# Performance work log

Hardware: AMD Instinct MI355X
Metric: run time of the kernel (lower is better)

## Reference

```python
import jax, jax.numpy as jnp
import numpy as np

# ---- constants (match init_kwargs) ----
H = 16            # bit depth of location codes
TP = 8            # number of parallel location dims
N = 1 << H        # location magnitude bound
N_K = 2
N_C = 2 * H * N_K + 1   # 65 candidate locations per token
T = 512           # T_train
N_TTNBR = 64
K_VOCAB = 128
S = N_TTNBR + K_VOCAB   # 192
D = 256           # dim_eu
TEMP = 0.05


def cos_similarity(c1, c2):
    """CritiGraph frexp-based cosine: sign product * (1 - bitlength(|a|^|b| + 1)/h)."""
    sg = (2 * (c1 >= 0).astype(jnp.int32) - 1) * (2 * (c2 >= 0).astype(jnp.int32) - 1)
    x = jnp.abs(c1) ^ jnp.abs(c2)
    _, e = jnp.frexp((x + 1).astype(jnp.float32))  # exponent == bit_length(x+1)
    return sg.astype(jnp.float32) * (1.0 - e.astype(jnp.float32) / H)


def setup_inputs() -> dict:
    key = jax.random.key(0)
    ks = jax.random.split(key, 8)
    loc = lambda k, shape: jax.random.randint(k, shape, 1 - N, N, dtype=jnp.int32)
    return {
        "cur_tar": jax.random.randint(ks[0], (T,), 0, K_VOCAB, dtype=jnp.int32),
        "cnc_loc": loc(ks[1], (T, N_C, TP)),
        "sta_loc": loc(ks[2], (T, TP)),
        "ttn_loc": loc(ks[3], (T, N_TTNBR, TP)),
        "voc_loc": loc(ks[4], (T, K_VOCAB, TP)),
        "sta_emb": 0.1 * jax.random.normal(ks[5], (T, D), dtype=jnp.float32),
        "ttn_emb": 0.1 * jax.random.normal(ks[6], (T, N_TTNBR, D), dtype=jnp.float32),
        "voc_emb": 0.1 * jax.random.normal(ks[7], (T, K_VOCAB, D), dtype=jnp.float32),
    }


def reference(cur_tar, cnc_loc, sta_loc, ttn_loc, voc_loc, sta_emb, ttn_emb, voc_emb):
    # positives = dynamic neighbors ++ sampled vocab
    pos_loc = jnp.concatenate([ttn_loc, voc_loc], axis=1)      # (T, S, TP) int32
    pos_emb = jnp.concatenate([ttn_emb, voc_emb], axis=1)      # (T, S, D)

    # Euclidean-space logits
    eu_val = 20.0 * TEMP * jnp.einsum('td,tsd->ts', sta_emb, pos_emb)  # (T, S)

    # CT-space similarities
    cos_sp = cos_similarity(sta_loc[:, None, :], pos_loc)      # (T, S, TP)
    cos_sum = cos_sp.sum(axis=-1)                              # (T, S)
    # candidate location swapped into each track d (ct_val_triton math)
    cos_cp = cos_similarity(cnc_loc[:, None, :, :], pos_loc[:, :, None, :])  # (T, S, N_C, TP)
    ct_val = (cos_sum[:, :, None, None] - cos_sp[:, :, None, :] + cos_cp) / TP \
             * (20.0 * TEMP)                                   # (T, S, N_C, TP)

    # KL(eu || ct) over the dynamic neighbors
    logits_ct_dyn = ct_val[:, :N_TTNBR]                        # (T, Nn, N_C, TP)
    logits_eu_dyn = eu_val[:, :N_TTNBR]                        # (T, Nn)
    p_eu = jax.nn.softmax(logits_eu_dyn, axis=1)
    lp_eu = jax.nn.log_softmax(logits_eu_dyn, axis=1)
    lp_ct = jax.nn.log_softmax(logits_ct_dyn, axis=1)
    loss_dyn_dyn = (p_eu[:, :, None, None] * (lp_eu[:, :, None, None] - lp_ct)).sum(axis=1)  # (T, N_C, TP)

    # cross-entropy over the sampled vocab
    logits_ct_sta = ct_val[:, N_TTNBR:] / TEMP                 # (T, K, N_C, TP)
    logits_flat = logits_ct_sta.reshape(T, K_VOCAB, N_C * TP)
    log_probs = jax.nn.log_softmax(logits_flat, axis=1)        # (T, K, N_C*TP)
    idx = jnp.broadcast_to(cur_tar[:, None, None].astype(jnp.int32), (T, 1, N_C * TP))
    target_lp = jnp.take_along_axis(log_probs, idx, axis=1)[:, 0, :]  # (T, N_C*TP)
    loss_dyn_sta = -target_lp.reshape(T, N_C, TP)              # (T, N_C, TP)

    return loss_dyn_dyn, loss_dyn_sta
```

## Files before the change

### kernel.cpp

```cpp
#include <hip/hip_runtime.h>


#define Tn   512
#define NC   65
#define TPd  8
#define NTn  64
#define KV   128
#define Sn   192
#define Dn   256
#define OUT1 (Tn * NC * TPd)

#define LOG2E 1.44269504088896340736f
#define LN2   0.69314718055994530942f
#define K1D (0.0625f * 0.125f * LOG2E)
#define K0D (-0.125f * LOG2E)
#define K1S (0.0625f * 2.5f * LOG2E)
#define K0S (-2.5f * LOG2E)

__device__ __forceinline__ float exp2_fast(float x) {
#if __has_builtin(__builtin_amdgcn_exp2f)
    return __builtin_amdgcn_exp2f(x);
#else
    return exp2f(x);
#endif
}
__device__ __forceinline__ int pack_loc(int v) {
    return (v < 0) ? (int)(0x80000000u | (unsigned)(-v)) : v;
}
__device__ __forceinline__ float asf(int v) { return __int_as_float(v); }

__device__ __forceinline__ float cos_cc(int y, float k1, float k0) {
    int   x  = (y & 0x7fffffff) + 1;
    float cc = fmaf((float)__clz(x), k1, k0);
    return __int_as_float(__float_as_int(cc) ^ (y & 0x80000000));
}

__global__ __launch_bounds__(256, 2) void critigraph_kernel(
    const int*   __restrict__ cur_tar,
    const int*   __restrict__ cnc_loc,
    const int*   __restrict__ sta_loc,
    const int*   __restrict__ ttn_loc,
    const int*   __restrict__ voc_loc,
    const float* __restrict__ sta_emb,
    const float* __restrict__ ttn_emb,
    float*       __restrict__ out)
{
    __shared__ int4  s_dyn4[NTn * TPd];
    __shared__ int2  s_sta2[KV * TPd];
    __shared__ int   s_cnc[NC * TPd];
    __shared__ int   s_staloc[TPd];
    __shared__ float s_csum[Sn];
    __shared__ float s_eu[NTn];
    __shared__ float s_peu[NTn];
    __shared__ float s_dotbase[TPd];
    __shared__ float s_kl;

    const int t   = blockIdx.x;
    const int tid = threadIdx.x;

    if (tid < TPd) s_staloc[tid] = pack_loc(sta_loc[t * TPd + tid]);
    for (int i = tid; i < NC * TPd; i += 256)
        s_cnc[i] = pack_loc(cnc_loc[t * NC * TPd + i]);
    __syncthreads();

    const int mysta = s_staloc[tid & 7];
    float mysp[6];
    #pragma unroll
    for (int k = 0; k < 6; ++k) {
        int i = tid + 256 * k;
        int s = i >> 3;
        int v = (s < NTn) ? ttn_loc[t * NTn * TPd + i]
                          : voc_loc[t * KV * TPd + (i - NTn * TPd)];
        int packed = pack_loc(v);
        int y = packed ^ mysta;
        int x = (y & 0x7fffffff) + 1;
        float c = fmaf((float)__clz(x), 0.0625f, -1.0f);
        c = __int_as_float(__float_as_int(c) ^ (y & 0x80000000));
        mysp[k] = c;
        if (s < NTn) s_dyn4[i].x = packed;
        else         s_sta2[i - NTn * TPd].x = packed;
        float v8 = c;
        v8 += __shfl_xor(v8, 1);
        v8 += __shfl_xor(v8, 2);
        v8 += __shfl_xor(v8, 4);
        if ((tid & 7) == 0) s_csum[s] = v8;
    }
    {
        const int r = tid >> 2, q = tid & 3;
        const float4* A = (const float4*)(sta_emb + (size_t)t * Dn);
        const float4* B = (const float4*)(ttn_emb + ((size_t)t * NTn + r) * Dn);
        float acc = 0.f;
        #pragma unroll
        for (int k = 0; k < 16; ++k) {
            float4 a = A[k * 4 + q];
            float4 b = B[k * 4 + q];
            acc += a.x * b.x + a.y * b.y + a.z * b.z + a.w * b.w;
        }
        acc += __shfl_xor(acc, 1);
        acc += __shfl_xor(acc, 2);
        if (q == 0) s_eu[r] = acc;
    }
    __syncthreads();

    #pragma unroll
    for (int k = 0; k < 6; ++k) {
        int i = tid + 256 * k;
        int s = i >> 3;
        float sc = (s < NTn) ? (0.125f * LOG2E) : (2.5f * LOG2E);
        float b2 = (s_csum[s] - mysp[k]) * sc;
        if (s < NTn) s_dyn4[i].y = __float_as_int(b2);
        else         s_sta2[i - NTn * TPd].y = __float_as_int(b2);
    }
    if (tid < 64) {
        float e  = s_eu[tid];
        float mx = e;
        #pragma unroll
        for (int m = 1; m < 64; m <<= 1) mx = fmaxf(mx, __shfl_xor(mx, m));
        float ex = __expf(e - mx);
        float z  = ex;
        #pragma unroll
        for (int m = 1; m < 64; m <<= 1) z += __shfl_xor(z, m);
        float pe = ex / z;
        s_peu[tid] = pe;
        float kls = pe * ((e - mx) - __logf(z));
        #pragma unroll
        for (int m = 1; m < 64; m <<= 1) kls += __shfl_xor(kls, m);
        if (tid == 0) s_kl = kls;
    }
    __syncthreads();

    #pragma unroll
    for (int k = 0; k < 2; ++k) {
        int i = tid + 256 * k;
        s_dyn4[i].z = __float_as_int(s_peu[i >> 3]);
    }
    if (tid < 64) {
        int g = tid & 7, j = tid >> 3;
        float a = 0.f;
        #pragma unroll
        for (int k = 0; k < 8; ++k) {
            int s = 8 * j + k;
            a = fmaf(s_peu[s], asf(s_dyn4[s * TPd + g].y), a);
        }
        #pragma unroll
        for (int m = 8; m < 64; m <<= 1) a += __shfl_xor(a, m);
        if (tid < TPd) s_dotbase[g] = a;
    }
    __syncthreads();

    const int p     = tid & 7;
    const int acnc1 = s_cnc[tid];
    const int acnc2 = s_cnc[tid + 256];
    const int tar   = cur_tar[t];
    const float kl  = s_kl;
    const float dtb = s_dotbase[p];

    float sumA = 0.f, dotA = 0.f, sumB = 0.f, dotB = 0.f;
    #pragma unroll 16
    for (int s = 0; s < NTn; ++s) {
        int4  ab = s_dyn4[s * TPd + p];
        float bb = asf(ab.y);
        float pe = asf(ab.z);
        float ccA = cos_cc(ab.x ^ acnc1, K1D, K0D);
        sumA += exp2_fast(bb + ccA);
        dotA  = fmaf(pe, ccA, dotA);
        float ccB = cos_cc(ab.x ^ acnc2, K1D, K0D);
        sumB += exp2_fast(bb + ccB);
        dotB  = fmaf(pe, ccB, dotB);
    }
    float s2A = 0.f, s2B = 0.f;
    #pragma unroll 16
    for (int v = 0; v < KV; ++v) {
        int2  ab = s_sta2[v * TPd + p];
        float bb = asf(ab.y);
        s2A += exp2_fast(bb + cos_cc(ab.x ^ acnc1, K1S, K0S));
        s2B += exp2_fast(bb + cos_cc(ab.x ^ acnc2, K1S, K0S));
    }
    {
        int2  tt = s_sta2[tar * TPd + p];
        float bt = asf(tt.y);
        float tA = bt + cos_cc(tt.x ^ acnc1, K1S, K0S);
        float tB = bt + cos_cc(tt.x ^ acnc2, K1S, K0S);
        float* od = out + (size_t)t * NC * TPd;
        float* os = out + OUT1 + (size_t)t * NC * TPd;
        od[tid]       = kl + LN2 * (__log2f(sumA) - (dtb + dotA));
        od[tid + 256] = kl + LN2 * (__log2f(sumB) - (dtb + dotB));
        os[tid]       = LN2 * (__log2f(s2A) - tA);
        os[tid + 256] = LN2 * (__log2f(s2B) - tB);
    }

    {
        const int w    = tid >> 6;
        const int lane = tid & 63;
        const int half = lane >> 5;
        const int sub  = lane & 31;
        const int pt   = 2 * w + half;
        const int acnct = s_cnc[512 + pt];
        float sumd = 0.f, dotd = 0.f, sums = 0.f;
        #pragma unroll
        for (int k = 0; k < 2; ++k) {
            int4 ab = s_dyn4[(sub + 32 * k) * TPd + pt];
            float cc = cos_cc(ab.x ^ acnct, K1D, K0D);
            sumd += exp2_fast(asf(ab.y) + cc);
            dotd  = fmaf(asf(ab.z), cc, dotd);
        }
        #pragma unroll
        for (int k = 0; k < 4; ++k) {
            int2 ab = s_sta2[(sub + 32 * k) * TPd + pt];
            sums += exp2_fast(asf(ab.y) + cos_cc(ab.x ^ acnct, K1S, K0S));
        }
        #pragma unroll
        for (int m = 1; m < 32; m <<= 1) {
            sumd += __shfl_xor(sumd, m);
            dotd += __shfl_xor(dotd, m);
            sums += __shfl_xor(sums, m);
        }
        if (sub == 0) {
            int2  tt = s_sta2[tar * TPd + pt];
            float tT = asf(tt.y) + cos_cc(tt.x ^ acnct, K1S, K0S);
            out[(size_t)t * NC * TPd + 512 + pt] =
                kl + LN2 * (__log2f(sumd) - (s_dotbase[pt] + dotd));
            out[OUT1 + (size_t)t * NC * TPd + 512 + pt] =
                LN2 * (__log2f(sums) - tT);
        }
    }
}

extern "C" void kernel_launch(void* const* d_in, const int* in_sizes, int n_in,
                              void* d_out, int out_size, void* d_ws, size_t ws_size,
                              hipStream_t stream) {
    (void)in_sizes; (void)n_in; (void)d_ws; (void)ws_size; (void)out_size;
    const int*   cur_tar = (const int*)  d_in[0];
    const int*   cnc_loc = (const int*)  d_in[1];
    const int*   sta_loc = (const int*)  d_in[2];
    const int*   ttn_loc = (const int*)  d_in[3];
    const int*   voc_loc = (const int*)  d_in[4];
    const float* sta_emb = (const float*)d_in[5];
    const float* ttn_emb = (const float*)d_in[6];
    critigraph_kernel<<<Tn, 256, 0, stream>>>(cur_tar, cnc_loc, sta_loc, ttn_loc,
                                              voc_loc, sta_emb, ttn_emb, (float*)d_out);
}
```

Before: 142.8 us.

## Replace per-element exp2 with shared lookup table and double block size

Factors exp2(b + cc) into exp2(b)*exp2(cc). The base exp2 is precomputed once per position, and exp2(cc) comes from a small shared-memory table indexed by clz and sign. The table is replicated 32 ways to avoid bank conflicts. Blocks grow to 512 threads so each thread handles one candidate column instead of two. This removes transcendental ops from the inner loops, at the cost of extra shared memory, table-fill work and table lookups, and it changes occupancy. The target log-prob term is recomputed from the cosine terms because stored values are now exponentiated.

```diff
diff --git a/kernel.cpp b/kernel.cpp
--- a/kernel.cpp
+++ b/kernel.cpp
@@ -9,11 +9,11 @@
 #define Sn   192
 #define Dn   256
 #define OUT1 (Tn * NC * TPd)
+#define TABN 34
+#define TABR (TABN * 32)
 
 #define LOG2E 1.44269504088896340736f
 #define LN2   0.69314718055994530942f
-#define K1D (0.0625f * 0.125f * LOG2E)
-#define K0D (-0.125f * LOG2E)
 #define K1S (0.0625f * 2.5f * LOG2E)
 #define K0S (-2.5f * LOG2E)
 
@@ -29,13 +29,18 @@
 }
 __device__ __forceinline__ float asf(int v) { return __int_as_float(v); }
 
-__device__ __forceinline__ float cos_cc(int y, float k1, float k0) {
-    int   x  = (y & 0x7fffffff) + 1;
-    float cc = fmaf((float)__clz(x), k1, k0);
-    return __int_as_float(__float_as_int(cc) ^ (y & 0x80000000));
-}
-
-__global__ __launch_bounds__(256, 2) void critigraph_kernel(
+__device__ __forceinline__ float cos_raw(int y) {
+    int   x = (y & 0x7fffffff) + 1;
+    float c = fmaf((float)__clz(x), 0.0625f, -1.0f);
+    return __int_as_float(__float_as_int(c) ^ (y & 0x80000000));
+}
+__device__ __forceinline__ int tab_idx(int y) {
+    int x = (y & 0x7fffffff) + 1;
+    int u = __clz(x) - 15;
+    return u * 2 + (int)(((unsigned)y) >> 31);
+}
+
+__global__ __launch_bounds__(512, 4) void critigraph_kernel(
     const int*   __restrict__ cur_tar,
     const int*   __restrict__ cnc_loc,
     const int*   __restrict__ sta_loc,
@@ -47,6 +52,7 @@
 {
     __shared__ int4  s_dyn4[NTn * TPd];
     __shared__ int2  s_sta2[KV * TPd];
+    __shared__ float s_tab[3 * TABR];
     __shared__ int   s_cnc[NC * TPd];
     __shared__ int   s_staloc[TPd];
     __shared__ float s_csum[Sn];
@@ -59,23 +65,31 @@
     const int tid = threadIdx.x;
 
     if (tid < TPd) s_staloc[tid] = pack_loc(sta_loc[t * TPd + tid]);
-    for (int i = tid; i < NC * TPd; i += 256)
+    for (int i = tid; i < NC * TPd; i += 512)
         s_cnc[i] = pack_loc(cnc_loc[t * NC * TPd + i]);
+    for (int i = tid; i < TABR; i += 512) {
+        int   idx = i >> 5;
+        int   clz = 15 + (idx >> 1);
+        float mag = (float)clz * 0.0625f - 1.0f;
+        float sgn = (idx & 1) ? -1.f : 1.f;
+        float ccd = sgn * mag * (0.125f * LOG2E);
+        float ccs = sgn * mag * (2.5f * LOG2E);
+        s_tab[i]            = exp2_fast(ccd);
+        s_tab[i + TABR]     = ccd;
+        s_tab[i + 2 * TABR] = exp2_fast(ccs);
+    }
     __syncthreads();
 
     const int mysta = s_staloc[tid & 7];
-    float mysp[6];
+    float mysp[3];
     #pragma unroll
-    for (int k = 0; k < 6; ++k) {
-        int i = tid + 256 * k;
+    for (int k = 0; k < 3; ++k) {
+        int i = tid + 512 * k;
         int s = i >> 3;
         int v = (s < NTn) ? ttn_loc[t * NTn * TPd + i]
                           : voc_loc[t * KV * TPd + (i - NTn * TPd)];
         int packed = pack_loc(v);
-        int y = packed ^ mysta;
-        int x = (y & 0x7fffffff) + 1;
-        float c = fmaf((float)__clz(x), 0.0625f, -1.0f);
-        c = __int_as_float(__float_as_int(c) ^ (y & 0x80000000));
+        float c = cos_raw(packed ^ mysta);
         mysp[k] = c;
         if (s < NTn) s_dyn4[i].x = packed;
         else         s_sta2[i - NTn * TPd].x = packed;
@@ -86,30 +100,35 @@
         if ((tid & 7) == 0) s_csum[s] = v8;
     }
     {
-        const int r = tid >> 2, q = tid & 3;
+        const int r = tid >> 3, q = tid & 7;
         const float4* A = (const float4*)(sta_emb + (size_t)t * Dn);
         const float4* B = (const float4*)(ttn_emb + ((size_t)t * NTn + r) * Dn);
         float acc = 0.f;
         #pragma unroll
-        for (int k = 0; k < 16; ++k) {
-            float4 a = A[k * 4 + q];
-            float4 b = B[k * 4 + q];
+        for (int k = 0; k < 8; ++k) {
+            float4 a = A[k * 8 + q];
+            float4 b = B[k * 8 + q];
             acc += a.x * b.x + a.y * b.y + a.z * b.z + a.w * b.w;
         }
         acc += __shfl_xor(acc, 1);
         acc += __shfl_xor(acc, 2);
+        acc += __shfl_xor(acc, 4);
         if (q == 0) s_eu[r] = acc;
     }
     __syncthreads();
 
     #pragma unroll
-    for (int k = 0; k < 6; ++k) {
-        int i = tid + 256 * k;
+    for (int k = 0; k < 3; ++k) {
+        int i = tid + 512 * k;
         int s = i >> 3;
-        float sc = (s < NTn) ? (0.125f * LOG2E) : (2.5f * LOG2E);
-        float b2 = (s_csum[s] - mysp[k]) * sc;
-        if (s < NTn) s_dyn4[i].y = __float_as_int(b2);
-        else         s_sta2[i - NTn * TPd].y = __float_as_int(b2);
+        if (s < NTn) {
+            float b2 = (s_csum[s] - mysp[k]) * (0.125f * LOG2E);
+            s_dyn4[i].y = __float_as_int(exp2_fast(b2));
+            s_dyn4[i].w = __float_as_int(b2);
+        } else {
+            float b2 = (s_csum[s] - mysp[k]) * (2.5f * LOG2E);
+            s_sta2[i - NTn * TPd].y = __float_as_int(exp2_fast(b2));
+        }
     }
     if (tid < 64) {
         float e  = s_eu[tid];
@@ -129,18 +148,14 @@
     }
     __syncthreads();
 
-    #pragma unroll
-    for (int k = 0; k < 2; ++k) {
-        int i = tid + 256 * k;
-        s_dyn4[i].z = __float_as_int(s_peu[i >> 3]);
-    }
+    s_dyn4[tid].z = __float_as_int(s_peu[tid >> 3]);
     if (tid < 64) {
         int g = tid & 7, j = tid >> 3;
         float a = 0.f;
         #pragma unroll
         for (int k = 0; k < 8; ++k) {
             int s = 8 * j + k;
-            a = fmaf(s_peu[s], asf(s_dyn4[s * TPd + g].y), a);
+            a = fmaf(s_peu[s], asf(s_dyn4[s * TPd + g].w), a);
         }
         #pragma unroll
         for (int m = 8; m < 64; m <<= 1) a += __shfl_xor(a, m);
@@ -148,80 +163,80 @@
     }
     __syncthreads();
 
-    const int p     = tid & 7;
-    const int acnc1 = s_cnc[tid];
-    const int acnc2 = s_cnc[tid + 256];
-    const int tar   = cur_tar[t];
-    const float kl  = s_kl;
-    const float dtb = s_dotbase[p];
-
-    float sumA = 0.f, dotA = 0.f, sumB = 0.f, dotB = 0.f;
+    const int   p    = tid & 7;
+    const int   acnc = s_cnc[tid];
+    const int   tar  = cur_tar[t];
+    const float kl   = s_kl;
+    const float dtb  = s_dotbase[p];
+    const float* tb  = s_tab + (tid & 31);
+
+    float sum = 0.f, dot = 0.f;
     #pragma unroll 16
     for (int s = 0; s < NTn; ++s) {
-        int4  ab = s_dyn4[s * TPd + p];
-        float bb = asf(ab.y);
-        float pe = asf(ab.z);
-        float ccA = cos_cc(ab.x ^ acnc1, K1D, K0D);
-        sumA += exp2_fast(bb + ccA);
-        dotA  = fmaf(pe, ccA, dotA);
-        float ccB = cos_cc(ab.x ^ acnc2, K1D, K0D);
-        sumB += exp2_fast(bb + ccB);
-        dotB  = fmaf(pe, ccB, dotB);
-    }
-    float s2A = 0.f, s2B = 0.f;
+        int4  ab  = s_dyn4[s * TPd + p];
+        int   j   = tab_idx(ab.x ^ acnc) * 32;
+        float eD  = tb[j];
+        float ccD = tb[j + TABR];
+        sum = fmaf(asf(ab.y), eD, sum);
+        dot = fmaf(asf(ab.z), ccD, dot);
+    }
+    float s2 = 0.f;
     #pragma unroll 16
     for (int v = 0; v < KV; ++v) {
         int2  ab = s_sta2[v * TPd + p];
-        float bb = asf(ab.y);
-        s2A += exp2_fast(bb + cos_cc(ab.x ^ acnc1, K1S, K0S));
-        s2B += exp2_fast(bb + cos_cc(ab.x ^ acnc2, K1S, K0S));
+        int   j  = tab_idx(ab.x ^ acnc) * 32;
+        s2 = fmaf(asf(ab.y), tb[j + 2 * TABR], s2);
     }
     {
-        int2  tt = s_sta2[tar * TPd + p];
-        float bt = asf(tt.y);
-        float tA = bt + cos_cc(tt.x ^ acnc1, K1S, K0S);
-        float tB = bt + cos_cc(tt.x ^ acnc2, K1S, K0S);
+        int   ax  = s_sta2[tar * TPd + p].x;
+        float sp  = cos_raw(ax ^ s_staloc[p]);
+        float b2t = (s_csum[NTn + tar] - sp) * (2.5f * LOG2E);
+        int   y   = ax ^ acnc;
+        int   x   = (y & 0x7fffffff) + 1;
+        float cct = fmaf((float)__clz(x), K1S, K0S);
+        cct = __int_as_float(__float_as_int(cct) ^ (y & 0x80000000));
         float* od = out + (size_t)t * NC * TPd;
         float* os = out + OUT1 + (size_t)t * NC * TPd;
-        od[tid]       = kl + LN2 * (__log2f(sumA) - (dtb + dotA));
-        od[tid + 256] = kl + LN2 * (__log2f(sumB) - (dtb + dotB));
-        os[tid]       = LN2 * (__log2f(s2A) - tA);
-        os[tid + 256] = LN2 * (__log2f(s2B) - tB);
+        od[tid] = kl + LN2 * (__log2f(sum) - (dtb + dot));
+        os[tid] = LN2 * (__log2f(s2) - (b2t + cct));
     }
 
     {
         const int w    = tid >> 6;
         const int lane = tid & 63;
-        const int half = lane >> 5;
-        const int sub  = lane & 31;
-        const int pt   = 2 * w + half;
-        const int acnct = s_cnc[512 + pt];
-        float sumd = 0.f, dotd = 0.f, sums = 0.f;
-        #pragma unroll
-        for (int k = 0; k < 2; ++k) {
-            int4 ab = s_dyn4[(sub + 32 * k) * TPd + pt];
-            float cc = cos_cc(ab.x ^ acnct, K1D, K0D);
-            sumd += exp2_fast(asf(ab.y) + cc);
-            dotd  = fmaf(asf(ab.z), cc, dotd);
-        }
-        #pragma unroll
-        for (int k = 0; k < 4; ++k) {
-            int2 ab = s_sta2[(sub + 32 * k) * TPd + pt];
-            sums += exp2_fast(asf(ab.y) + cos_cc(ab.x ^ acnct, K1S, K0S));
-        }
-        #pragma unroll
-        for (int m = 1; m < 32; m <<= 1) {
+        const int acw  = s_cnc[512 + w];
+        float sumd, dotd, sums;
+        {
+            int4  ab = s_dyn4[lane * TPd + w];
+            int   j  = tab_idx(ab.x ^ acw) * 32;
+            sumd = asf(ab.y) * tb[j];
+            dotd = asf(ab.z) * tb[j + TABR];
+        }
+        {
+            int2 ab0 = s_sta2[lane * TPd + w];
+            int2 ab1 = s_sta2[(lane + 64) * TPd + w];
+            int  j0  = tab_idx(ab0.x ^ acw) * 32;
+            int  j1  = tab_idx(ab1.x ^ acw) * 32;
+            sums = asf(ab0.y) * tb[j0 + 2 * TABR] + asf(ab1.y) * tb[j1 + 2 * TABR];
+        }
+        #pragma unroll
+        for (int m = 1; m < 64; m <<= 1) {
             sumd += __shfl_xor(sumd, m);
             dotd += __shfl_xor(dotd, m);
             sums += __shfl_xor(sums, m);
         }
-        if (sub == 0) {
-            int2  tt = s_sta2[tar * TPd + pt];
-            float tT = asf(tt.y) + cos_cc(tt.x ^ acnct, K1S, K0S);
-            out[(size_t)t * NC * TPd + 512 + pt] =
-                kl + LN2 * (__log2f(sumd) - (s_dotbase[pt] + dotd));
-            out[OUT1 + (size_t)t * NC * TPd + 512 + pt] =
-                LN2 * (__log2f(sums) - tT);
+        if (lane == 0) {
+            int   ax  = s_sta2[tar * TPd + w].x;
+            float sp  = cos_raw(ax ^ s_staloc[w]);
+            float b2t = (s_csum[NTn + tar] - sp) * (2.5f * LOG2E);
+            int   y   = ax ^ acw;
+            int   x   = (y & 0x7fffffff) + 1;
+            float cct = fmaf((float)__clz(x), K1S, K0S);
+            cct = __int_as_float(__float_as_int(cct) ^ (y & 0x80000000));
+            out[(size_t)t * NC * TPd + 512 + w] =
+                kl + LN2 * (__log2f(sumd) - (s_dotbase[w] + dotd));
+            out[OUT1 + (size_t)t * NC * TPd + 512 + w] =
+                LN2 * (__log2f(sums) - (b2t + cct));
         }
     }
 }
@@ -237,6 +252,6 @@
     const int*   voc_loc = (const int*)  d_in[4];
     const float* sta_emb = (const float*)d_in[5];
     const float* ttn_emb = (const float*)d_in[6];
-    critigraph_kernel<<<Tn, 256, 0, stream>>>(cur_tar, cnc_loc, sta_loc, ttn_loc,
+    critigraph_kernel<<<Tn, 512, 0, stream>>>(cur_tar, cnc_loc, sta_loc, ttn_loc,
                                               voc_loc, sta_emb, ttn_emb, (float*)d_out);
 }
```

After: 143.5 us. No clear change (+0.4%).
